# Optimization experiments

Measured on AMD Instinct MI355X. Metric: run time of the kernel, lower is better.

The kernel has to match this reference:

```python
import jax, jax.numpy as jnp
import numpy as np

N = 8192      # num_nodes
B = 16        # batch
IN_DIM = 2    # input_dim
HID = 64      # hid_dim
K = 2         # diffusion_steps
DEG = 16
E = N * DEG
F = IN_DIM + HID            # concat(input, state) feature dim
NUM_MAT = 2 * K + 1         # dual random walk: 2 matrices * K steps + identity


def _spmm(vals, rows, cols, x):
    # sparse [N,N] @ dense [N,M]: y[rows[e]] += vals[e] * x[cols[e]]
    return jax.ops.segment_sum(vals[:, None] * x[cols], rows, num_segments=N)


def _diff_conv(x, W, b, edge_src, edge_dst, vals1, vals2):
    # x: [B, N, F] -> [B, N*out_dim]; Chebyshev-like diffusion recursion
    x0 = jnp.transpose(x, (1, 2, 0)).reshape(N, F * B)  # [N, F*B]
    xs = [x0]
    # matrix 1 = D_out^-1 A (edges src->dst), matrix 2 = D_in^-1 A^T (edges dst->src)
    for rows, cols, vals in ((edge_src, edge_dst, vals1), (edge_dst, edge_src, vals2)):
        x1 = _spmm(vals, rows, cols, x0)
        xs.append(x1)
        xp, xc = x0, x1
        for _ in range(2, K + 1):
            xn = 2.0 * _spmm(vals, rows, cols, xc) - xp
            xs.append(xn)
            xp, xc = xc, xn
    xstk = jnp.stack(xs, 0).reshape(NUM_MAT, N, F, B)
    xstk = jnp.transpose(xstk, (3, 1, 2, 0)).reshape(B * N, F * NUM_MAT)
    out = xstk @ W + b  # [B*N, out_dim]
    return out.reshape(B, -1)


def setup_inputs() -> dict:
    key = jax.random.key(0)
    k = jax.random.split(key, 8)
    inputs = jax.random.normal(k[0], (B, N * IN_DIM), jnp.float32)
    state = jax.random.normal(k[1], (B, N * HID), jnp.float32)
    edge_src = jax.random.randint(k[2], (E,), 0, N)
    edge_dst = jax.random.randint(k[3], (E,), 0, N)
    a = jax.random.uniform(k[4], (E,), jnp.float32) + 0.1  # positive edge weights
    dout = jax.ops.segment_sum(a, edge_src, num_segments=N)
    din = jax.ops.segment_sum(a, edge_dst, num_segments=N)
    vals1 = a / jnp.where(dout > 0, dout, 1.0)[edge_src]  # random-walk normalize A
    vals2 = a / jnp.where(din > 0, din, 1.0)[edge_dst]    # random-walk normalize A^T
    std_g = 1.414 * np.sqrt(2.0 / (F * NUM_MAT + 2 * HID)).astype(np.float32)
    std_c = 1.414 * np.sqrt(2.0 / (F * NUM_MAT + HID)).astype(np.float32)
    W_gate = jax.random.normal(k[5], (F * NUM_MAT, 2 * HID), jnp.float32) * std_g
    b_gate = jnp.zeros((2 * HID,), jnp.float32)
    W_cand = jax.random.normal(k[6], (F * NUM_MAT, HID), jnp.float32) * std_c
    b_cand = jnp.zeros((HID,), jnp.float32)
    return dict(inputs=inputs, state=state, edge_src=edge_src, edge_dst=edge_dst,
                vals1=vals1, vals2=vals2, W_gate=W_gate, b_gate=b_gate,
                W_cand=W_cand, b_cand=b_cand)


def reference(inputs, state, edge_src, edge_dst, vals1, vals2,
              W_gate, b_gate, W_cand, b_cand):
    i = inputs.reshape(B, N, IN_DIM)
    s = state.reshape(B, N, HID)
    x = jnp.concatenate([i, s], axis=2)  # [B, N, F]
    value = jax.nn.sigmoid(_diff_conv(x, W_gate, b_gate, edge_src, edge_dst, vals1, vals2))
    value = value.reshape(B, N, 2 * HID)
    r = value[..., :HID].reshape(B, N * HID)
    u = value[..., HID:].reshape(B, N * HID)
    rs = (r * state).reshape(B, N, HID)
    xc = jnp.concatenate([i, rs], axis=2)
    c = jnp.tanh(_diff_conv(xc, W_cand, b_cand, edge_src, edge_dst, vals1, vals2))
    new_state = u * state + (1.0 - u) * c
    return (new_state, new_state)
```

## Files before the change

### kernel.cpp

```cpp
#include <hip/hip_runtime.h>
#include <cstddef>
#include <cstdint>

#define NNODES 8192
#define BATCH  16
#define HID    64
#define NEDGE  131072
#define SN     524288
#define OUTHALF 8388608
#define FP2    72
#define SLABU  1152
#define NSTR   5760
#define NSTR4  720
#define XCS4   144
#define KP2    384
#define GN     4

typedef __attribute__((ext_vector_type(8))) short bf16x8;
typedef __attribute__((ext_vector_type(4))) float f32x4;

static __device__ __forceinline__ float bf2f(ushort u) {
    union { uint32_t i; float f; } c; c.i = ((uint32_t)u) << 16; return c.f;
}
static __device__ __forceinline__ ushort f2bf(float f) {
    union { float f; uint32_t i; } c; c.f = f;
    uint32_t lsb = (c.i >> 16) & 1;
    return (ushort)((c.i + 0x7fffu + lsb) >> 16);
}


__global__ void zero_counts_kernel(int* __restrict__ c1, int* __restrict__ c2) {
    int i = blockIdx.x * 256 + threadIdx.x;
    if (i < NNODES) { c1[i] = 0; c2[i] = 0; }
}

__global__ void hist_kernel(const int* __restrict__ src, const int* __restrict__ dst,
                            int* __restrict__ c1, int* __restrict__ c2) {
    int e = blockIdx.x * 256 + threadIdx.x;
    if (e < NEDGE) {
        atomicAdd(&c1[src[e]], 1);
        atomicAdd(&c2[dst[e]], 1);
    }
}

__global__ __launch_bounds__(1024) void scan_kernel(const int* __restrict__ counts,
                                                    int* __restrict__ rowptr,
                                                    int* __restrict__ cursor) {
    __shared__ int sh[1024];
    int tid = threadIdx.x;
    int base = tid * 8;
    int local[8];
    int sum = 0;
#pragma unroll
    for (int j = 0; j < 8; ++j) { local[j] = counts[base + j]; sum += local[j]; }
    sh[tid] = sum;
    __syncthreads();
    for (int off = 1; off < 1024; off <<= 1) {
        int v = (tid >= off) ? sh[tid - off] : 0;
        __syncthreads();
        sh[tid] += v;
        __syncthreads();
    }
    int p = sh[tid] - sum;
#pragma unroll
    for (int j = 0; j < 8; ++j) {
        cursor[base + j] = p;
        p += local[j];
        rowptr[base + j + 1] = p;
    }
    if (tid == 0) rowptr[0] = 0;
}

__global__ void scatter_kernel(const int* __restrict__ src, const int* __restrict__ dst,
                               const float* __restrict__ v1, const float* __restrict__ v2,
                               int* __restrict__ cur1, int* __restrict__ cur2,
                               int* __restrict__ cols1, float* __restrict__ valsC1,
                               int* __restrict__ cols2, float* __restrict__ valsC2) {
    int e = blockIdx.x * 256 + threadIdx.x;
    if (e < NEDGE) {
        int r1 = src[e];
        int p1 = atomicAdd(&cur1[r1], 1);
        cols1[p1] = dst[e];
        valsC1[p1] = v1[e];
        int r2 = dst[e];
        int p2 = atomicAdd(&cur2[r2], 1);
        cols2[p2] = src[e];
        valsC2[p2] = v2[e];
    }
}


__global__ void convert_w_kernel(const float* __restrict__ Wg, const float* __restrict__ Wc,
                                 ushort* __restrict__ WgT, ushort* __restrict__ WcT) {
    int i = blockIdx.x * 256 + threadIdx.x;
    if (i >= 192 * KP2) return;
    int col = i / KP2, k2 = i - col * KP2;
    int m = k2 / FP2, f = k2 - m * FP2;
    bool valid = (m < 5) && (f < 66);
    int ko = f * 5 + m;
    if (col < 128) {
        WgT[col * KP2 + k2] = valid ? f2bf(Wg[ko * 128 + col]) : (ushort)0;
    } else {
        int c = col - 128;
        WcT[c * KP2 + k2] = valid ? f2bf(Wc[ko * 64 + c]) : (ushort)0;
    }
}


__global__ void build_x0_kernel(const float* __restrict__ inputs, const float* __restrict__ state,
                                uint* __restrict__ Xb_u, uint* __restrict__ Xc_u) {
    int t = blockIdx.x * 256 + threadIdx.x;
    if (t >= NNODES * BATCH * 36) return;
    int n = t / 576;
    int r = t - n * 576;
    int b = r / 36;
    int j = r - b * 36;
    int f0 = 2 * j;
    uint val = 0;
    if (f0 == 0) {
        float v0 = inputs[(size_t)b * (NNODES * 2) + n * 2 + 0];
        float v1 = inputs[(size_t)b * (NNODES * 2) + n * 2 + 1];
        val = (uint)f2bf(v0) | ((uint)f2bf(v1) << 16);
    } else if (f0 < 66) {
        float v0 = state[(size_t)b * SN + n * HID + (f0 - 2)];
        float v1 = state[(size_t)b * SN + n * HID + (f0 - 1)];
        val = (uint)f2bf(v0) | ((uint)f2bf(v1) << 16);
    }
    Xb_u[(size_t)n * 2880 + r] = val;
    if (f0 == 0 || f0 >= 66) Xc_u[t] = val;
}


static __device__ __forceinline__ void fma8(float* acc, uint4 d, float v) {
    acc[0] += v * bf2f((ushort)(d.x));  acc[1] += v * bf2f((ushort)(d.x >> 16));
    acc[2] += v * bf2f((ushort)(d.y));  acc[3] += v * bf2f((ushort)(d.y >> 16));
    acc[4] += v * bf2f((ushort)(d.z));  acc[5] += v * bf2f((ushort)(d.z >> 16));
    acc[6] += v * bf2f((ushort)(d.w));  acc[7] += v * bf2f((ushort)(d.w >> 16));
}

static __device__ __forceinline__ uint4 blend_pack8(const float* acc, uint4 p,
                                                    float alpha, float beta) {
    float o[8];
    o[0] = alpha * acc[0] + beta * bf2f((ushort)(p.x));
    o[1] = alpha * acc[1] + beta * bf2f((ushort)(p.x >> 16));
    o[2] = alpha * acc[2] + beta * bf2f((ushort)(p.y));
    o[3] = alpha * acc[3] + beta * bf2f((ushort)(p.y >> 16));
    o[4] = alpha * acc[4] + beta * bf2f((ushort)(p.z));
    o[5] = alpha * acc[5] + beta * bf2f((ushort)(p.z >> 16));
    o[6] = alpha * acc[6] + beta * bf2f((ushort)(p.w));
    o[7] = alpha * acc[7] + beta * bf2f((ushort)(p.w >> 16));
    uint4 r;
    r.x = (uint32_t)f2bf(o[0]) | ((uint32_t)f2bf(o[1]) << 16);
    r.y = (uint32_t)f2bf(o[2]) | ((uint32_t)f2bf(o[3]) << 16);
    r.z = (uint32_t)f2bf(o[4]) | ((uint32_t)f2bf(o[5]) << 16);
    r.w = (uint32_t)f2bf(o[6]) | ((uint32_t)f2bf(o[7]) << 16);
    return r;
}

__global__ __launch_bounds__(128) void spmm_dual(
        const int* __restrict__ rp1, const int* __restrict__ c1, const float* __restrict__ v1,
        const uint4* __restrict__ x1,
        const int* __restrict__ rp2, const int* __restrict__ c2, const float* __restrict__ v2,
        const uint4* __restrict__ x2,
        int xs,
        const uint4* __restrict__ xp, int ps,
        uint4* __restrict__ y1, uint4* __restrict__ y2, int ys,
        float alpha, float beta) {
    int bid = blockIdx.x;
    int half = bid >> 13;
    int n = bid & 8191;
    const int* rowptr = half ? rp2 : rp1;
    const int* cols   = half ? c2 : c1;
    const float* vals = half ? v2 : v1;
    const uint4* x    = half ? x2 : x1;
    uint4* y          = half ? y2 : y1;

    int t = threadIdx.x;
    int s = rowptr[n], e = rowptr[n + 1];
    float a0[8] = {0, 0, 0, 0, 0, 0, 0, 0};
    float a1[8] = {0, 0, 0, 0, 0, 0, 0, 0};
    bool tail = t < 16;
    int t2 = 128 + t;
    int i = s;
    for (; i + 4 <= e; i += 4) {
        int cA = cols[i], cB = cols[i + 1], cC = cols[i + 2], cD = cols[i + 3];
        float vA = vals[i], vB = vals[i + 1], vC = vals[i + 2], vD = vals[i + 3];
        const uint4* rA = x + (size_t)cA * xs;
        const uint4* rB = x + (size_t)cB * xs;
        const uint4* rC = x + (size_t)cC * xs;
        const uint4* rD = x + (size_t)cD * xs;
        uint4 dA = rA[t], dB = rB[t], dC = rC[t], dD = rD[t];
        uint4 eA, eB, eC, eD;
        if (tail) { eA = rA[t2]; eB = rB[t2]; eC = rC[t2]; eD = rD[t2]; }
        fma8(a0, dA, vA); fma8(a0, dB, vB); fma8(a0, dC, vC); fma8(a0, dD, vD);
        if (tail) { fma8(a1, eA, vA); fma8(a1, eB, vB); fma8(a1, eC, vC); fma8(a1, eD, vD); }
    }
    for (; i < e; ++i) {
        int cA = cols[i];
        float vA = vals[i];
        const uint4* rA = x + (size_t)cA * xs;
        uint4 dA = rA[t];
        if (tail) { uint4 dA1 = rA[t2]; fma8(a1, dA1, vA); }
        fma8(a0, dA, vA);
    }
    uint4* yb = y + (size_t)n * ys;
    const uint4* xpb = xp + (size_t)n * ps;
    uint4 p0 = (beta != 0.f) ? xpb[t] : make_uint4(0, 0, 0, 0);
    yb[t] = blend_pack8(a0, p0, alpha, beta);
    if (tail) {
        uint4 p1 = (beta != 0.f) ? xpb[t2] : make_uint4(0, 0, 0, 0);
        yb[t2] = blend_pack8(a1, p1, alpha, beta);
    }
}


__global__ __launch_bounds__(256, 4) void gate_mfma(const ushort* __restrict__ Xb,
                                                    const ushort* __restrict__ WgT,
                                                    const float* __restrict__ bg,
                                                    const float* __restrict__ state,
                                                    float* __restrict__ U,
                                                    ushort* __restrict__ Xc) {
    int tid = threadIdx.x;
    int wave = tid >> 6, lane = tid & 63;
    int row = lane & 15, quad = lane >> 4;
    int c0 = wave * 32 + row;
    int c1 = c0 + 16;

    bf16x8 w0[12], w1[12];
#pragma unroll
    for (int kt = 0; kt < 12; ++kt) {
        w0[kt] = *(const bf16x8*)(WgT + (size_t)c0 * KP2 + kt * 32 + quad * 8);
        w1[kt] = *(const bf16x8*)(WgT + (size_t)c1 * KP2 + kt * 32 + quad * 8);
    }
    float bias0 = bg[c0], bias1 = bg[c1];

    int offA[11];
#pragma unroll
    for (int kt = 0; kt < 11; ++kt) {
        int j = 4 * kt + quad;
        int m = j / 9;
        int f0 = 8 * (j - 9 * m);
        offA[kt] = m * SLABU + row * FP2 + f0;
    }
    int off11 = 4 * SLABU + row * FP2 + 64;

    int nodeBase = blockIdx.x * GN;
    for (int g = 0; g < GN; ++g) {
        int n = nodeBase + g;
        const ushort* An = Xb + (size_t)n * NSTR;
        f32x4 acc0 = {0.f, 0.f, 0.f, 0.f};
        f32x4 acc1 = {0.f, 0.f, 0.f, 0.f};
#pragma unroll
        for (int kt = 0; kt < 11; ++kt) {
            bf16x8 av = *(const bf16x8*)(An + offA[kt]);
            acc0 = __builtin_amdgcn_mfma_f32_16x16x32_bf16(av, w0[kt], acc0, 0, 0, 0);
            acc1 = __builtin_amdgcn_mfma_f32_16x16x32_bf16(av, w1[kt], acc1, 0, 0, 0);
        }
        {
            bf16x8 av = {0, 0, 0, 0, 0, 0, 0, 0};
            if (quad == 0) av = *(const bf16x8*)(An + off11);
            acc0 = __builtin_amdgcn_mfma_f32_16x16x32_bf16(av, w0[11], acc0, 0, 0, 0);
            acc1 = __builtin_amdgcn_mfma_f32_16x16x32_bf16(av, w1[11], acc1, 0, 0, 0);
        }
#pragma unroll
        for (int r = 0; r < 4; ++r) {
            int b = quad * 4 + r;
            float v0 = 1.f / (1.f + __expf(-(acc0[r] + bias0)));
            float v1 = 1.f / (1.f + __expf(-(acc1[r] + bias1)));
            if (wave < 2) {
                float s0 = state[(size_t)b * SN + n * HID + c0];
                float s1 = state[(size_t)b * SN + n * HID + c1];
                Xc[(size_t)n * SLABU + b * FP2 + 2 + c0] = f2bf(v0 * s0);
                Xc[(size_t)n * SLABU + b * FP2 + 2 + c1] = f2bf(v1 * s1);
            } else {
                U[(size_t)b * SN + n * HID + (c0 - HID)] = v0;
                U[(size_t)b * SN + n * HID + (c1 - HID)] = v1;
            }
        }
    }
}


__global__ __launch_bounds__(256, 4) void cand_mfma(const ushort* __restrict__ Xb,
                                                    const ushort* __restrict__ Xc,
                                                    const ushort* __restrict__ WcT,
                                                    const float* __restrict__ bc,
                                                    const float* __restrict__ state,
                                                    const float* U,
                                                    float* out) {
    int tid = threadIdx.x;
    int wave = tid >> 6, lane = tid & 63;
    int row = lane & 15, quad = lane >> 4;
    int c = wave * 16 + row;

    bf16x8 w[12];
#pragma unroll
    for (int kt = 0; kt < 12; ++kt)
        w[kt] = *(const bf16x8*)(WcT + (size_t)c * KP2 + kt * 32 + quad * 8);
    float bias = bc[c];

    int offA[11];
#pragma unroll
    for (int kt = 0; kt < 11; ++kt) {
        int j = 4 * kt + quad;
        int m = j / 9;
        int f0 = 8 * (j - 9 * m);
        offA[kt] = m * SLABU + row * FP2 + f0;
    }
    int off11 = 4 * SLABU + row * FP2 + 64;

    int nodeBase = blockIdx.x * GN;
    for (int g = 0; g < GN; ++g) {
        int n = nodeBase + g;
        const ushort* AnB = Xb + (size_t)n * NSTR;
        const ushort* AnC = Xc + (size_t)n * SLABU;
        f32x4 acc = {0.f, 0.f, 0.f, 0.f};
#pragma unroll
        for (int kt = 0; kt < 11; ++kt) {
            const ushort* bp = (kt < 2) ? AnC
                             : (kt == 2 ? (quad == 0 ? AnC : AnB) : AnB);
            bf16x8 av = *(const bf16x8*)(bp + offA[kt]);
            acc = __builtin_amdgcn_mfma_f32_16x16x32_bf16(av, w[kt], acc, 0, 0, 0);
        }
        {
            bf16x8 av = {0, 0, 0, 0, 0, 0, 0, 0};
            if (quad == 0) av = *(const bf16x8*)(AnB + off11);
            acc = __builtin_amdgcn_mfma_f32_16x16x32_bf16(av, w[11], acc, 0, 0, 0);
        }
#pragma unroll
        for (int r = 0; r < 4; ++r) {
            int b = quad * 4 + r;
            float pre = acc[r] + bias;
            float cv = 1.f - 2.f / (__expf(2.f * pre) + 1.f);
            size_t idx = (size_t)b * SN + n * HID + c;
            float uv = U[idx];
            float s = state[idx];
            float ns = uv * s + (1.f - uv) * cv;
            out[idx] = ns;
            out[OUTHALF + idx] = ns;
        }
    }
}


extern "C" void kernel_launch(void* const* d_in, const int* in_sizes, int n_in,
                              void* d_out, int out_size, void* d_ws, size_t ws_size,
                              hipStream_t stream) {
    const float* inputs = (const float*)d_in[0];
    const float* state  = (const float*)d_in[1];
    const int*   esrc   = (const int*)d_in[2];
    const int*   edst   = (const int*)d_in[3];
    const float* v1     = (const float*)d_in[4];
    const float* v2     = (const float*)d_in[5];
    const float* Wg     = (const float*)d_in[6];
    const float* bg     = (const float*)d_in[7];
    const float* Wc     = (const float*)d_in[8];
    const float* bc     = (const float*)d_in[9];
    float* out = (float*)d_out;

    char* ws = (char*)d_ws;
    size_t off = 0;
    auto alloc = [&](size_t bytes) -> void* {
        void* p = ws + off;
        off += (bytes + 255) & ~(size_t)255;
        return p;
    };
    ushort* Xb     = (ushort*)alloc((size_t)NNODES * NSTR * 2);
    ushort* Xc     = (ushort*)alloc((size_t)NNODES * SLABU * 2);
    ushort* WgT    = (ushort*)alloc((size_t)128 * KP2 * 2);
    ushort* WcT    = (ushort*)alloc((size_t)64 * KP2 * 2);
    int*   counts1 = (int*)alloc(NNODES * 4);
    int*   counts2 = (int*)alloc(NNODES * 4);
    int*   rowptr1 = (int*)alloc((NNODES + 1) * 4);
    int*   rowptr2 = (int*)alloc((NNODES + 1) * 4);
    int*   cursor1 = (int*)alloc(NNODES * 4);
    int*   cursor2 = (int*)alloc(NNODES * 4);
    int*   cols1   = (int*)alloc(NEDGE * 4);
    int*   cols2   = (int*)alloc(NEDGE * 4);
    float* valsC1  = (float*)alloc(NEDGE * 4);
    float* valsC2  = (float*)alloc(NEDGE * 4);

    float* U = out + OUTHALF;

    uint4* Xb4 = (uint4*)Xb;
    uint4* Xc4 = (uint4*)Xc;
    auto slab = [&](int m) { return Xb4 + (size_t)m * 144; };

    zero_counts_kernel<<<(NNODES + 255) / 256, 256, 0, stream>>>(counts1, counts2);
    hist_kernel<<<(NEDGE + 255) / 256, 256, 0, stream>>>(esrc, edst, counts1, counts2);
    scan_kernel<<<1, 1024, 0, stream>>>(counts1, rowptr1, cursor1);
    scan_kernel<<<1, 1024, 0, stream>>>(counts2, rowptr2, cursor2);
    scatter_kernel<<<(NEDGE + 255) / 256, 256, 0, stream>>>(esrc, edst, v1, v2,
                                                            cursor1, cursor2,
                                                            cols1, valsC1, cols2, valsC2);

    convert_w_kernel<<<(192 * KP2 + 255) / 256, 256, 0, stream>>>(Wg, Wc, WgT, WcT);
    build_x0_kernel<<<(NNODES * BATCH * 36 + 255) / 256, 256, 0, stream>>>(
        inputs, state, (uint*)Xb, (uint*)Xc);

    spmm_dual<<<2 * NNODES, 128, 0, stream>>>(rowptr1, cols1, valsC1, slab(0),
                                              rowptr2, cols2, valsC2, slab(0), NSTR4,
                                              slab(0), NSTR4, slab(1), slab(3), NSTR4,
                                              1.f, 0.f);
    spmm_dual<<<2 * NNODES, 128, 0, stream>>>(rowptr1, cols1, valsC1, slab(1),
                                              rowptr2, cols2, valsC2, slab(3), NSTR4,
                                              slab(0), NSTR4, slab(2), slab(4), NSTR4,
                                              2.f, -1.f);

    gate_mfma<<<NNODES / GN, 256, 0, stream>>>(Xb, WgT, bg, state, U, Xc);

    spmm_dual<<<2 * NNODES, 128, 0, stream>>>(rowptr1, cols1, valsC1, Xc4,
                                              rowptr2, cols2, valsC2, Xc4, XCS4,
                                              Xc4, XCS4, slab(1), slab(3), NSTR4,
                                              1.f, 0.f);
    spmm_dual<<<2 * NNODES, 128, 0, stream>>>(rowptr1, cols1, valsC1, slab(1),
                                              rowptr2, cols2, valsC2, slab(3), NSTR4,
                                              Xc4, XCS4, slab(2), slab(4), NSTR4,
                                              2.f, -1.f);

    cand_mfma<<<NNODES / GN, 256, 0, stream>>>(Xb, Xc, WcT, bc, state, U, out);
}
```

Measured before the change: 603.5 us.

## Split SpMM rows into eight feature slices with edge-parallel wave groups

The dual SpMM kernel moves from one 128-thread block per row to eight 64-thread blocks per row, each covering 18 uint4 columns of the 144-wide row. Within a block, three groups of 18 lanes handle different edges, and partial sums are combined with shuffles. The aim is to raise parallelism and memory-level concurrency on the gather-bound SpMM and to remove the tail-thread imbalance. The cost is 8x more blocks, 10 idle lanes per wave, and repeated reads of rowptr, cols and vals for every slice. The gate and candidate MFMA kernels also drop launch_bounds min-blocks from 4 to 2, allowing more registers per thread.

New measurement: 629.0 us. 4.2% more time.

```diff
diff --git a/kernel.cpp b/kernel.cpp
--- a/kernel.cpp
+++ b/kernel.cpp
@@ -157,7 +157,7 @@
     return r;
 }
 
-__global__ __launch_bounds__(128) void spmm_dual(
+__global__ __launch_bounds__(64) void spmm_dual8(
         const int* __restrict__ rp1, const int* __restrict__ c1, const float* __restrict__ v1,
         const uint4* __restrict__ x1,
         const int* __restrict__ rp2, const int* __restrict__ c2, const float* __restrict__ v2,
@@ -167,54 +167,51 @@
         uint4* __restrict__ y1, uint4* __restrict__ y2, int ys,
         float alpha, float beta) {
     int bid = blockIdx.x;
-    int half = bid >> 13;
-    int n = bid & 8191;
-    const int* rowptr = half ? rp2 : rp1;
-    const int* cols   = half ? c2 : c1;
-    const float* vals = half ? v2 : v1;
-    const uint4* x    = half ? x2 : x1;
-    uint4* y          = half ? y2 : y1;
+    int slice = bid & 7;
+    int pair  = bid >> 3;
+    int n     = pair & 8191;
+    int graph = pair >> 13;
+    const int* rowptr = graph ? rp2 : rp1;
+    const int* cols   = graph ? c2 : c1;
+    const float* vals = graph ? v2 : v1;
+    const uint4* x    = graph ? x2 : x1;
+    uint4* y          = graph ? y2 : y1;
 
     int t = threadIdx.x;
+    int eg = t / 18;
+    int li = t - eg * 18;
+    int base = slice * 18 + li;
+    bool active = t < 54;
     int s = rowptr[n], e = rowptr[n + 1];
-    float a0[8] = {0, 0, 0, 0, 0, 0, 0, 0};
-    float a1[8] = {0, 0, 0, 0, 0, 0, 0, 0};
-    bool tail = t < 16;
-    int t2 = 128 + t;
-    int i = s;
-    for (; i + 4 <= e; i += 4) {
-        int cA = cols[i], cB = cols[i + 1], cC = cols[i + 2], cD = cols[i + 3];
-        float vA = vals[i], vB = vals[i + 1], vC = vals[i + 2], vD = vals[i + 3];
-        const uint4* rA = x + (size_t)cA * xs;
-        const uint4* rB = x + (size_t)cB * xs;
-        const uint4* rC = x + (size_t)cC * xs;
-        const uint4* rD = x + (size_t)cD * xs;
-        uint4 dA = rA[t], dB = rB[t], dC = rC[t], dD = rD[t];
-        uint4 eA, eB, eC, eD;
-        if (tail) { eA = rA[t2]; eB = rB[t2]; eC = rC[t2]; eD = rD[t2]; }
-        fma8(a0, dA, vA); fma8(a0, dB, vB); fma8(a0, dC, vC); fma8(a0, dD, vD);
-        if (tail) { fma8(a1, eA, vA); fma8(a1, eB, vB); fma8(a1, eC, vC); fma8(a1, eD, vD); }
-    }
-    for (; i < e; ++i) {
-        int cA = cols[i];
-        float vA = vals[i];
-        const uint4* rA = x + (size_t)cA * xs;
-        uint4 dA = rA[t];
-        if (tail) { uint4 dA1 = rA[t2]; fma8(a1, dA1, vA); }
-        fma8(a0, dA, vA);
-    }
-    uint4* yb = y + (size_t)n * ys;
-    const uint4* xpb = xp + (size_t)n * ps;
-    uint4 p0 = (beta != 0.f) ? xpb[t] : make_uint4(0, 0, 0, 0);
-    yb[t] = blend_pack8(a0, p0, alpha, beta);
-    if (tail) {
-        uint4 p1 = (beta != 0.f) ? xpb[t2] : make_uint4(0, 0, 0, 0);
-        yb[t2] = blend_pack8(a1, p1, alpha, beta);
-    }
-}
-
-
-__global__ __launch_bounds__(256, 4) void gate_mfma(const ushort* __restrict__ Xb,
+    float acc[8] = {0, 0, 0, 0, 0, 0, 0, 0};
+    const uint4 uz = make_uint4(0, 0, 0, 0);
+    for (int i = s; i < e; i += 6) {
+        int iA = i + eg, iB = i + 3 + eg;
+        bool okA = active && (iA < e);
+        bool okB = active && (iB < e);
+        int cA  = okA ? cols[iA] : 0;
+        int cB  = okB ? cols[iB] : 0;
+        float vA = okA ? vals[iA] : 0.f;
+        float vB = okB ? vals[iB] : 0.f;
+        uint4 dA = okA ? x[(size_t)cA * xs + base] : uz;
+        uint4 dB = okB ? x[(size_t)cB * xs + base] : uz;
+        fma8(acc, dA, vA);
+        fma8(acc, dB, vB);
+    }
+#pragma unroll
+    for (int j = 0; j < 8; ++j) {
+        float a18 = __shfl(acc[j], t + 18);
+        float a36 = __shfl(acc[j], t + 36);
+        acc[j] += a18 + a36;
+    }
+    if (t < 18) {
+        uint4 p = (beta != 0.f) ? xp[(size_t)n * ps + base] : uz;
+        y[(size_t)n * ys + base] = blend_pack8(acc, p, alpha, beta);
+    }
+}
+
+
+__global__ __launch_bounds__(256, 2) void gate_mfma(const ushort* __restrict__ Xb,
                                                     const ushort* __restrict__ WgT,
                                                     const float* __restrict__ bg,
                                                     const float* __restrict__ state,
@@ -281,7 +278,7 @@
 }
 
 
-__global__ __launch_bounds__(256, 4) void cand_mfma(const ushort* __restrict__ Xb,
+__global__ __launch_bounds__(256, 2) void cand_mfma(const ushort* __restrict__ Xb,
                                                     const ushort* __restrict__ Xc,
                                                     const ushort* __restrict__ WcT,
                                                     const float* __restrict__ bc,
@@ -398,25 +395,27 @@
     build_x0_kernel<<<(NNODES * BATCH * 36 + 255) / 256, 256, 0, stream>>>(
         inputs, state, (uint*)Xb, (uint*)Xc);
 
-    spmm_dual<<<2 * NNODES, 128, 0, stream>>>(rowptr1, cols1, valsC1, slab(0),
-                                              rowptr2, cols2, valsC2, slab(0), NSTR4,
-                                              slab(0), NSTR4, slab(1), slab(3), NSTR4,
-                                              1.f, 0.f);
-    spmm_dual<<<2 * NNODES, 128, 0, stream>>>(rowptr1, cols1, valsC1, slab(1),
-                                              rowptr2, cols2, valsC2, slab(3), NSTR4,
-                                              slab(0), NSTR4, slab(2), slab(4), NSTR4,
-                                              2.f, -1.f);
+    const int SPG = 2 * NNODES * 8;
+
+    spmm_dual8<<<SPG, 64, 0, stream>>>(rowptr1, cols1, valsC1, slab(0),
+                                       rowptr2, cols2, valsC2, slab(0), NSTR4,
+                                       slab(0), NSTR4, slab(1), slab(3), NSTR4,
+                                       1.f, 0.f);
+    spmm_dual8<<<SPG, 64, 0, stream>>>(rowptr1, cols1, valsC1, slab(1),
+                                       rowptr2, cols2, valsC2, slab(3), NSTR4,
+                                       slab(0), NSTR4, slab(2), slab(4), NSTR4,
+                                       2.f, -1.f);
 
     gate_mfma<<<NNODES / GN, 256, 0, stream>>>(Xb, WgT, bg, state, U, Xc);
 
-    spmm_dual<<<2 * NNODES, 128, 0, stream>>>(rowptr1, cols1, valsC1, Xc4,
-                                              rowptr2, cols2, valsC2, Xc4, XCS4,
-                                              Xc4, XCS4, slab(1), slab(3), NSTR4,
-                                              1.f, 0.f);
-    spmm_dual<<<2 * NNODES, 128, 0, stream>>>(rowptr1, cols1, valsC1, slab(1),
-                                              rowptr2, cols2, valsC2, slab(3), NSTR4,
-                                              Xc4, XCS4, slab(2), slab(4), NSTR4,
-                                              2.f, -1.f);
+    spmm_dual8<<<SPG, 64, 0, stream>>>(rowptr1, cols1, valsC1, Xc4,
+                                       rowptr2, cols2, valsC2, Xc4, XCS4,
+                                       Xc4, XCS4, slab(1), slab(3), NSTR4,
+                                       1.f, 0.f);
+    spmm_dual8<<<SPG, 64, 0, stream>>>(rowptr1, cols1, valsC1, slab(1),
+                                       rowptr2, cols2, valsC2, slab(3), NSTR4,
+                                       Xc4, XCS4, slab(2), slab(4), NSTR4,
+                                       2.f, -1.f);
 
     cand_mfma<<<NNODES / GN, 256, 0, stream>>>(Xb, Xc, WcT, bc, state, U, out);
 }
```
